# Kernel optimization log

Measured on AMD Instinct MI355X. Metric: run time of the kernel, lower is better.

Reference implementation:

```python
import jax, jax.numpy as jnp
import numpy as np

NUM_USERS = 100000
NUM_ITEMS = 50000
N = NUM_USERS + NUM_ITEMS  # total nodes
DIM = 64                   # dim_h
E = 2000000                # number of edges
NUM_LAYERS = 2


def setup_inputs() -> dict:
    key = jax.random.key(0)
    k0, k1, k2, k3, k4 = jax.random.split(key, 5)
    edge_index = jax.random.randint(k0, (2, E), 0, N, dtype=jnp.int64)
    edge_weight = jax.random.uniform(k1, (E,), dtype=jnp.float32)
    # nn.init.normal_(std=0.01) embeddings
    emb_users = 0.01 * jax.random.normal(k2, (NUM_USERS, DIM), dtype=jnp.float32)
    emb_items = 0.01 * jax.random.normal(k3, (NUM_ITEMS, DIM), dtype=jnp.float32)
    # nn.Linear(dim_h, dim_h)
    kW, kb = jax.random.split(k4)
    bound = 1.0 / np.sqrt(DIM)
    W = jax.random.uniform(kW, (DIM, DIM), minval=-bound, maxval=bound, dtype=jnp.float32)
    b = jax.random.uniform(kb, (DIM,), minval=-bound, maxval=bound, dtype=jnp.float32)
    return {"edge_index": edge_index, "edge_weight": edge_weight,
            "emb_users": emb_users, "emb_items": emb_items, "W": W, "b": b}


def reference(edge_index, edge_weight, emb_users, emb_items, W, b):
    # emb = cat([user_emb, item_emb])  -> [N, DIM]
    emb = jnp.concatenate([emb_users, emb_items], axis=0)
    src, dst = edge_index[0], edge_index[1]
    acc = emb  # running sum over layer embeddings (embs list)
    for _ in range(NUM_LAYERS):
        # LGConv with edge_weight: out[i] = sum_{j->i} w * x[j], then .relu()
        msg = edge_weight[:, None] * emb[src]            # [E, DIM] gather
        emb = jax.nn.relu(jax.ops.segment_sum(msg, dst, num_segments=N))
        acc = acc + emb
    emb_final = acc / (NUM_LAYERS + 1)                   # mean over stacked embs
    emb_final = emb_final @ W.T + b                      # final linear
    emb_users_final = emb_final[:NUM_USERS]
    emb_items_final = emb_final[NUM_USERS:]
    return (emb_users_final, emb_users, emb_items_final, emb_items)
```

## Files before the change

### kernel.cpp

```cpp
#include <hip/hip_runtime.h>
#include <hip/hip_fp16.h>

#define NUSERS 100000
#define NITEMS 50000
#define NNODES (NUSERS + NITEMS)
#define DIM 64
#define NEDGE 2000000
#define FT_ROWS 128
#define FT_BLOCKS ((NNODES + FT_ROWS - 1) / FT_ROWS)

#define BSH 7
#define NB ((NNODES + 127) >> BSH)
#define CAP 2048
#define CHUNK 4096
#define ABLOCKS ((NEDGE + CHUNK - 1) / CHUNK)
#define CONVB ((NNODES * DIM / 4 + 511) / 512)

__global__ __launch_bounds__(512)
void bucketconv_kernel(const int* __restrict__ eidx, const float* __restrict__ ew,
                       int* __restrict__ gcur, int2* __restrict__ regions,
                       const float* __restrict__ eu, const float* __restrict__ eit,
                       __half* __restrict__ tbl) {
    const int t = threadIdx.x;

    if (blockIdx.x >= ABLOCKS) {
        long i = (long)(blockIdx.x - ABLOCKS) * 512 + t;
        const long total = (long)NNODES * DIM / 4;
        if (i < total) {
            const long ue = (long)NUSERS * DIM / 4;
            float4 v = (i < ue) ? ((const float4*)eu)[i] : ((const float4*)eit)[i - ue];
            ((__half2*)tbl)[2 * i + 0] = __floats2half2_rn(v.x, v.y);
            ((__half2*)tbl)[2 * i + 1] = __floats2half2_rn(v.z, v.w);
        }
        return;
    }

    __shared__ int cursor_s[NB];
    __shared__ int excl_s[NB];
    __shared__ int gbase_s[NB];
    __shared__ int scanbuf[512];
    __shared__ int2 stage[CHUNK];
    __shared__ unsigned short sbkt[CHUNK];

    const int e0 = blockIdx.x * CHUNK;
    const int cnt_edges = min(CHUNK, NEDGE - e0);

    for (int i = t; i < NB; i += 512) cursor_s[i] = 0;
    __syncthreads();

    int2 recs[8];
    int bk[8];
    const int e4base = e0 >> 2;
#pragma unroll
    for (int k = 0; k < 2; ++k) {
        int g = k * 512 + t;
        bool ok = (4 * g) < cnt_edges;
        int4 s4 = make_int4(0, 0, 0, 0), d4 = make_int4(0, 0, 0, 0);
        float4 w4 = make_float4(0.f, 0.f, 0.f, 0.f);
        if (ok) {
            int e4 = e4base + g;
            s4 = ((const int4*)eidx)[e4];
            d4 = ((const int4*)eidx)[(NEDGE >> 2) + e4];
            w4 = ((const float4*)ew)[e4];
        }
        int ss[4] = {s4.x, s4.y, s4.z, s4.w};
        int dd[4] = {d4.x, d4.y, d4.z, d4.w};
        float ww[4] = {w4.x, w4.y, w4.z, w4.w};
#pragma unroll
        for (int j = 0; j < 4; ++j) {
            int idx = 4 * k + j;
            if (ok) {
                int d = dd[j];
                int b = d >> BSH;
                bk[idx] = b;
                recs[idx].x = ss[j] | ((d & 127) << 18);
                recs[idx].y = __float_as_int(ww[j]);
                atomicAdd(&cursor_s[b], 1);
            } else {
                bk[idx] = -1;
            }
        }
    }
    __syncthreads();

    int myv[3];
    int tsum = 0;
    const int base_i = t * 3;
#pragma unroll
    for (int j = 0; j < 3; ++j) {
        int i = base_i + j;
        myv[j] = (i < NB) ? cursor_s[i] : 0;
        tsum += myv[j];
    }
    scanbuf[t] = tsum;
    __syncthreads();
    for (int d = 1; d < 512; d <<= 1) {
        int u = (t >= d) ? scanbuf[t - d] : 0;
        __syncthreads();
        scanbuf[t] += u;
        __syncthreads();
    }
    int run = scanbuf[t] - tsum;
#pragma unroll
    for (int j = 0; j < 3; ++j) {
        int i = base_i + j;
        if (i < NB) {
            excl_s[i] = run;
            cursor_s[i] = run;
            if (myv[j] > 0) gbase_s[i] = atomicAdd(&gcur[i], myv[j]);
            run += myv[j];
        }
    }
    __syncthreads();

#pragma unroll
    for (int k = 0; k < 8; ++k) {
        if (bk[k] >= 0) {
            int p = atomicAdd(&cursor_s[bk[k]], 1);
            stage[p] = recs[k];
            sbkt[p] = (unsigned short)bk[k];
        }
    }
    __syncthreads();

    for (int i = t; i < cnt_edges; i += 512) {
        int b = sbkt[i];
        int gpos = gbase_s[b] + (i - excl_s[b]);
        if (gpos < CAP) regions[(long)b * CAP + gpos] = stage[i];
    }
}

__global__ __launch_bounds__(512)
void sortpull1_kernel(const int* __restrict__ gcur, const int2* __restrict__ regions,
                      const __half* __restrict__ tbl,
                      int2* __restrict__ edge_sorted, int2* __restrict__ rs,
                      __half* __restrict__ buf1h) {
    __shared__ int2 srec[CAP];
    __shared__ int cnt[128];
    __shared__ int excl[128];
    __shared__ int scanbuf[128];
    const int t = threadIdx.x;
    const int b = blockIdx.x;
    const int node0 = b << BSH;
    const int ecnt = min(gcur[b], CAP);
    const long gbase = (long)b * CAP;

    if (t < 128) cnt[t] = 0;
    __syncthreads();

    int2 recs[4];
#pragma unroll
    for (int k = 0; k < 4; ++k) {
        int i = k * 512 + t;
        if (i < ecnt) {
            recs[k] = regions[gbase + i];
            atomicAdd(&cnt[(recs[k].x >> 18) & 127], 1);
        }
    }
    __syncthreads();

    if (t < 128) scanbuf[t] = cnt[t];
    __syncthreads();
    for (int d = 1; d < 128; d <<= 1) {
        int u = 0;
        if (t < 128 && t >= d) u = scanbuf[t - d];
        __syncthreads();
        if (t < 128) scanbuf[t] += u;
        __syncthreads();
    }
    if (t < 128) {
        excl[t] = scanbuf[t] - cnt[t];
        cnt[t] = scanbuf[t] - cnt[t];
    }
    __syncthreads();

#pragma unroll
    for (int k = 0; k < 4; ++k) {
        int i = k * 512 + t;
        if (i < ecnt) {
            int d = (recs[k].x >> 18) & 127;
            int p = atomicAdd(&cnt[d], 1);
            int2 o;
            o.x = recs[k].x & 0x3FFFF;
            o.y = recs[k].y;
            srec[p] = o;
        }
    }
    __syncthreads();

    for (int i = t; i < ecnt; i += 512) edge_sorted[gbase + i] = srec[i];
    if (t < 128) {
        int node = node0 + t;
        if (node < NNODES) {
            int2 p;
            p.x = (int)gbase + excl[t];
            p.y = (int)gbase + cnt[t];
            rs[node] = p;
        }
    }

    const int lane = t & 63;
    const int wv = t >> 6;
    const int g = lane >> 4;
    const int gl = lane & 15;
    const int2* tb4 = (const int2*)tbl;
#pragma unroll 1
    for (int j = 0; j < 16; ++j) {
        const int local = wv * 16 + j;
        const int node = node0 + local;
        if (node >= NNODES) break;
        int i = excl[local];
        const int iend = cnt[local];
        float4 acc = make_float4(0.f, 0.f, 0.f, 0.f);
        for (; i + 15 < iend; i += 16) {
#pragma unroll
            for (int u = 0; u < 4; ++u) {
                int2 r = srec[i + 4 * u + g];
                float w = __int_as_float(r.y);
                int2 hv = tb4[((long)r.x << 4) + gl];
                float2 f0 = __half22float2(*(const __half2*)&hv.x);
                float2 f1 = __half22float2(*(const __half2*)&hv.y);
                acc.x = fmaf(w, f0.x, acc.x); acc.y = fmaf(w, f0.y, acc.y);
                acc.z = fmaf(w, f1.x, acc.z); acc.w = fmaf(w, f1.y, acc.w);
            }
        }
        if (i < iend) {
#pragma unroll
            for (int u = 0; u < 4; ++u) {
                int idx = i + 4 * u + g;
                if (idx < iend) {
                    int2 r = srec[idx];
                    float w = __int_as_float(r.y);
                    int2 hv = tb4[((long)r.x << 4) + gl];
                    float2 f0 = __half22float2(*(const __half2*)&hv.x);
                    float2 f1 = __half22float2(*(const __half2*)&hv.y);
                    acc.x = fmaf(w, f0.x, acc.x); acc.y = fmaf(w, f0.y, acc.y);
                    acc.z = fmaf(w, f1.x, acc.z); acc.w = fmaf(w, f1.y, acc.w);
                }
            }
        }
        acc.x += __shfl_xor(acc.x, 16); acc.y += __shfl_xor(acc.y, 16);
        acc.z += __shfl_xor(acc.z, 16); acc.w += __shfl_xor(acc.w, 16);
        acc.x += __shfl_xor(acc.x, 32); acc.y += __shfl_xor(acc.y, 32);
        acc.z += __shfl_xor(acc.z, 32); acc.w += __shfl_xor(acc.w, 32);
        if (g == 0) {
            __half2 o0 = __floats2half2_rn(fmaxf(acc.x, 0.f), fmaxf(acc.y, 0.f));
            __half2 o1 = __floats2half2_rn(fmaxf(acc.z, 0.f), fmaxf(acc.w, 0.f));
            int2 ov;
            ov.x = *(const int*)&o0;
            ov.y = *(const int*)&o1;
            ((int2*)buf1h)[((long)node << 4) + gl] = ov;
        }
    }
}

__global__ __launch_bounds__(512)
void pull2_kernel(const int* __restrict__ gcur, const int2* __restrict__ rs,
                  const int2* __restrict__ edge_sorted,
                  const __half* __restrict__ in_emb,
                  __half* __restrict__ out_emb) {
    __shared__ int2 srec[CAP];
    __shared__ int2 rsl[128];
    const int t = threadIdx.x;
    const int b = blockIdx.x;
    const int node0 = b << BSH;
    const int ecnt = min(gcur[b], CAP);
    const long gbase = (long)b * CAP;

    for (int i = t; i < ecnt; i += 512) srec[i] = edge_sorted[gbase + i];
    if (t < 128) {
        int node = node0 + t;
        rsl[t] = (node < NNODES) ? rs[node] : make_int2(0, 0);
    }
    __syncthreads();

    const int lane = t & 63;
    const int wv = t >> 6;
    const int g = lane >> 4;
    const int gl = lane & 15;
    const int2* tb4 = (const int2*)in_emb;
#pragma unroll 1
    for (int j = 0; j < 16; ++j) {
        const int local = wv * 16 + j;
        const int node = node0 + local;
        if (node >= NNODES) break;
        int i = rsl[local].x - (int)gbase;
        const int iend = rsl[local].y - (int)gbase;
        float4 acc = make_float4(0.f, 0.f, 0.f, 0.f);
        for (; i + 15 < iend; i += 16) {
#pragma unroll
            for (int u = 0; u < 4; ++u) {
                int2 r = srec[i + 4 * u + g];
                float w = __int_as_float(r.y);
                int2 hv = tb4[((long)r.x << 4) + gl];
                float2 f0 = __half22float2(*(const __half2*)&hv.x);
                float2 f1 = __half22float2(*(const __half2*)&hv.y);
                acc.x = fmaf(w, f0.x, acc.x); acc.y = fmaf(w, f0.y, acc.y);
                acc.z = fmaf(w, f1.x, acc.z); acc.w = fmaf(w, f1.y, acc.w);
            }
        }
        if (i < iend) {
#pragma unroll
            for (int u = 0; u < 4; ++u) {
                int idx = i + 4 * u + g;
                if (idx < iend) {
                    int2 r = srec[idx];
                    float w = __int_as_float(r.y);
                    int2 hv = tb4[((long)r.x << 4) + gl];
                    float2 f0 = __half22float2(*(const __half2*)&hv.x);
                    float2 f1 = __half22float2(*(const __half2*)&hv.y);
                    acc.x = fmaf(w, f0.x, acc.x); acc.y = fmaf(w, f0.y, acc.y);
                    acc.z = fmaf(w, f1.x, acc.z); acc.w = fmaf(w, f1.y, acc.w);
                }
            }
        }
        acc.x += __shfl_xor(acc.x, 16); acc.y += __shfl_xor(acc.y, 16);
        acc.z += __shfl_xor(acc.z, 16); acc.w += __shfl_xor(acc.w, 16);
        acc.x += __shfl_xor(acc.x, 32); acc.y += __shfl_xor(acc.y, 32);
        acc.z += __shfl_xor(acc.z, 32); acc.w += __shfl_xor(acc.w, 32);
        if (g == 0) {
            __half2 o0 = __floats2half2_rn(fmaxf(acc.x, 0.f), fmaxf(acc.y, 0.f));
            __half2 o1 = __floats2half2_rn(fmaxf(acc.z, 0.f), fmaxf(acc.w, 0.f));
            int2 ov;
            ov.x = *(const int*)&o0;
            ov.y = *(const int*)&o1;
            ((int2*)out_emb)[((long)node << 4) + gl] = ov;
        }
    }
}

__global__ __launch_bounds__(256)
void final_kernel(const float* __restrict__ eu, const float* __restrict__ eit,
                  const __half* __restrict__ e1, const __half* __restrict__ e2,
                  const float* __restrict__ W, const float* __restrict__ bias,
                  float* __restrict__ out) {
    __shared__ float4 As4[FT_ROWS * 16];
    const int t = threadIdx.x;
    const int lane = t & 63;
    const int wv = t >> 6;
    const long R0 = (long)blockIdx.x * FT_ROWS;

    float wreg[64];
#pragma unroll
    for (int k = 0; k < 16; ++k) {
        float4 wq = ((const float4*)(W + (long)lane * 64))[k];
        wreg[4 * k + 0] = wq.x; wreg[4 * k + 1] = wq.y;
        wreg[4 * k + 2] = wq.z; wreg[4 * k + 3] = wq.w;
    }
    float bj = bias[lane];

#pragma unroll
    for (int it = 0; it < 8; ++it) {
        int idx = it * 256 + t;
        long row = R0 + (idx >> 4);
        if (row < NNODES) {
            int q = idx & 15;
            const float4* g0;
            long co;
            if (row < NUSERS) {
                g0 = (const float4*)(eu + (row << 6));
                co = (long)NUSERS * DIM + (row << 6);
            } else {
                g0 = (const float4*)(eit + ((row - NUSERS) << 6));
                co = (long)2 * NUSERS * DIM + (long)NITEMS * DIM + ((row - NUSERS) << 6);
            }
            float4 v0 = g0[q];
            ((float4*)(out + co))[q] = v0;
            const __half2* h1 = (const __half2*)(e1 + (row << 6));
            const __half2* h2 = (const __half2*)(e2 + (row << 6));
            float2 f1a = __half22float2(h1[2 * q]), f1b = __half22float2(h1[2 * q + 1]);
            float2 f2a = __half22float2(h2[2 * q]), f2b = __half22float2(h2[2 * q + 1]);
            float4 s;
            s.x = v0.x + f1a.x + f2a.x; s.y = v0.y + f1a.y + f2a.y;
            s.z = v0.z + f1b.x + f2b.x; s.w = v0.w + f1b.y + f2b.y;
            As4[idx] = s;
        }
    }
    __syncthreads();

#pragma unroll 4
    for (int r = 0; r < 32; ++r) {
        int tr = wv * 32 + r;
        long row = R0 + tr;
        if (row >= NNODES) break;
        const float4* a = As4 + tr * 16;
        float s0 = 0.f, s1 = 0.f;
#pragma unroll
        for (int k = 0; k < 16; ++k) {
            float4 v = a[k];
            s0 = fmaf(v.x, wreg[4 * k + 0], s0);
            s1 = fmaf(v.y, wreg[4 * k + 1], s1);
            s0 = fmaf(v.z, wreg[4 * k + 2], s0);
            s1 = fmaf(v.w, wreg[4 * k + 3], s1);
        }
        float val = fmaf(s0 + s1, (1.0f / 3.0f), bj);
        long o = (row < NUSERS) ? row * DIM
                                : (long)2 * NUSERS * DIM + (row - NUSERS) * DIM;
        out[o + lane] = val;
    }
}

extern "C" void kernel_launch(void* const* d_in, const int* in_sizes, int n_in,
                              void* d_out, int out_size, void* d_ws, size_t ws_size,
                              hipStream_t stream) {
    const int*   eidx = (const int*)d_in[0];
    const float* ew   = (const float*)d_in[1];
    const float* eu   = (const float*)d_in[2];
    const float* eit  = (const float*)d_in[3];
    const float* W    = (const float*)d_in[4];
    const float* bias = (const float*)d_in[5];
    float* out = (float*)d_out;

    const size_t nfeat = (size_t)NNODES * DIM;
    __half* tbl         = (__half*)d_ws;
    __half* buf1h       = tbl + nfeat;
    __half* buf2h       = buf1h + nfeat;
    int2*   regions     = (int2*)(buf2h + nfeat);
    int2*   edge_sorted = regions + (long)NB * CAP;
    int2*   rs          = edge_sorted + (long)NB * CAP;
    int*    gcur        = (int*)(rs + NNODES);

    hipMemsetAsync(gcur, 0, NB * sizeof(int), stream);

    bucketconv_kernel<<<ABLOCKS + CONVB, 512, 0, stream>>>(eidx, ew, gcur, regions,
                                                           eu, eit, tbl);

    sortpull1_kernel<<<NB, 512, 0, stream>>>(gcur, regions, tbl,
                                             edge_sorted, rs, buf1h);

    pull2_kernel<<<NB, 512, 0, stream>>>(gcur, rs, edge_sorted, buf1h, buf2h);

    final_kernel<<<FT_BLOCKS, 256, 0, stream>>>(eu, eit, buf1h, buf2h, W, bias, out);
}
```

Baseline: 339.1 us.

## Use fp16 MFMA for final linear and move passthrough copy to conversion kernel

Rewrites the final linear layer as 16-row MFMA tiles (f32_16x16x32_f16), with W converted to fp16 fragments in registers and the three layer embeddings summed in fp16 from the half tables. It drops the fp32 reload of the original embeddings and moves their passthrough copy into the earlier fp32-to-half conversion blocks. The aim is to cut final-kernel FMA work and fp32 memory traffic. In exchange the input sum is now formed in fp16, so precision is lower, and the output stores are scattered 4-byte writes.

```diff
diff --git a/kernel.cpp b/kernel.cpp
--- a/kernel.cpp
+++ b/kernel.cpp
@@ -6,8 +6,6 @@
 #define NNODES (NUSERS + NITEMS)
 #define DIM 64
 #define NEDGE 2000000
-#define FT_ROWS 128
-#define FT_BLOCKS ((NNODES + FT_ROWS - 1) / FT_ROWS)
 
 #define BSH 7
 #define NB ((NNODES + 127) >> BSH)
@@ -16,11 +14,17 @@
 #define ABLOCKS ((NEDGE + CHUNK - 1) / CHUNK)
 #define CONVB ((NNODES * DIM / 4 + 511) / 512)
 
+#define NTILES (NNODES / 16)
+#define FTB ((NTILES + 7) / 8)
+
+typedef _Float16 f16x8 __attribute__((ext_vector_type(8)));
+typedef float f32x4 __attribute__((ext_vector_type(4)));
+
 __global__ __launch_bounds__(512)
 void bucketconv_kernel(const int* __restrict__ eidx, const float* __restrict__ ew,
                        int* __restrict__ gcur, int2* __restrict__ regions,
                        const float* __restrict__ eu, const float* __restrict__ eit,
-                       __half* __restrict__ tbl) {
+                       __half* __restrict__ tbl, float* __restrict__ out) {
     const int t = threadIdx.x;
 
     if (blockIdx.x >= ABLOCKS) {
@@ -28,7 +32,15 @@
         const long total = (long)NNODES * DIM / 4;
         if (i < total) {
             const long ue = (long)NUSERS * DIM / 4;
-            float4 v = (i < ue) ? ((const float4*)eu)[i] : ((const float4*)eit)[i - ue];
+            float4 v;
+            if (i < ue) {
+                v = ((const float4*)eu)[i];
+                ((float4*)(out + (long)NUSERS * DIM))[i] = v;
+            } else {
+                long j = i - ue;
+                v = ((const float4*)eit)[j];
+                ((float4*)(out + (long)2 * NUSERS * DIM + (long)NITEMS * DIM))[j] = v;
+            }
             ((__half2*)tbl)[2 * i + 0] = __floats2half2_rn(v.x, v.y);
             ((__half2*)tbl)[2 * i + 1] = __floats2half2_rn(v.z, v.w);
         }
@@ -329,74 +341,65 @@
     }
 }
 
-__global__ __launch_bounds__(256)
-void final_kernel(const float* __restrict__ eu, const float* __restrict__ eit,
-                  const __half* __restrict__ e1, const __half* __restrict__ e2,
-                  const float* __restrict__ W, const float* __restrict__ bias,
-                  float* __restrict__ out) {
-    __shared__ float4 As4[FT_ROWS * 16];
+__global__ __launch_bounds__(512)
+void final_kernel(const __half* __restrict__ tbl, const __half* __restrict__ e1,
+                  const __half* __restrict__ e2, const float* __restrict__ W,
+                  const float* __restrict__ bias, float* __restrict__ out) {
     const int t = threadIdx.x;
     const int lane = t & 63;
     const int wv = t >> 6;
-    const long R0 = (long)blockIdx.x * FT_ROWS;
-
-    float wreg[64];
-#pragma unroll
-    for (int k = 0; k < 16; ++k) {
-        float4 wq = ((const float4*)(W + (long)lane * 64))[k];
-        wreg[4 * k + 0] = wq.x; wreg[4 * k + 1] = wq.y;
-        wreg[4 * k + 2] = wq.z; wreg[4 * k + 3] = wq.w;
-    }
-    float bj = bias[lane];
-
-#pragma unroll
-    for (int it = 0; it < 8; ++it) {
-        int idx = it * 256 + t;
-        long row = R0 + (idx >> 4);
-        if (row < NNODES) {
-            int q = idx & 15;
-            const float4* g0;
-            long co;
-            if (row < NUSERS) {
-                g0 = (const float4*)(eu + (row << 6));
-                co = (long)NUSERS * DIM + (row << 6);
-            } else {
-                g0 = (const float4*)(eit + ((row - NUSERS) << 6));
-                co = (long)2 * NUSERS * DIM + (long)NITEMS * DIM + ((row - NUSERS) << 6);
-            }
-            float4 v0 = g0[q];
-            ((float4*)(out + co))[q] = v0;
-            const __half2* h1 = (const __half2*)(e1 + (row << 6));
-            const __half2* h2 = (const __half2*)(e2 + (row << 6));
-            float2 f1a = __half22float2(h1[2 * q]), f1b = __half22float2(h1[2 * q + 1]);
-            float2 f2a = __half22float2(h2[2 * q]), f2b = __half22float2(h2[2 * q + 1]);
-            float4 s;
-            s.x = v0.x + f1a.x + f2a.x; s.y = v0.y + f1a.y + f2a.y;
-            s.z = v0.z + f1b.x + f2b.x; s.w = v0.w + f1b.y + f2b.y;
-            As4[idx] = s;
-        }
-    }
-    __syncthreads();
-
-#pragma unroll 4
-    for (int r = 0; r < 32; ++r) {
-        int tr = wv * 32 + r;
-        long row = R0 + tr;
-        if (row >= NNODES) break;
-        const float4* a = As4 + tr * 16;
-        float s0 = 0.f, s1 = 0.f;
-#pragma unroll
-        for (int k = 0; k < 16; ++k) {
-            float4 v = a[k];
-            s0 = fmaf(v.x, wreg[4 * k + 0], s0);
-            s1 = fmaf(v.y, wreg[4 * k + 1], s1);
-            s0 = fmaf(v.z, wreg[4 * k + 2], s0);
-            s1 = fmaf(v.w, wreg[4 * k + 3], s1);
-        }
-        float val = fmaf(s0 + s1, (1.0f / 3.0f), bj);
+    const int tile = blockIdx.x * 8 + wv;
+    if (tile >= NTILES) return;
+    const int m = lane & 15;
+    const int kg = lane >> 4;
+
+    f16x8 bfr[4][2];
+#pragma unroll
+    for (int nt = 0; nt < 4; ++nt) {
+#pragma unroll
+        for (int kh = 0; kh < 2; ++kh) {
+            const float4* wp = (const float4*)(W + (nt * 16 + m) * 64 + kh * 32 + kg * 8);
+            float4 w0 = wp[0], w1 = wp[1];
+            f16x8 bb;
+            bb[0] = (_Float16)w0.x; bb[1] = (_Float16)w0.y;
+            bb[2] = (_Float16)w0.z; bb[3] = (_Float16)w0.w;
+            bb[4] = (_Float16)w1.x; bb[5] = (_Float16)w1.y;
+            bb[6] = (_Float16)w1.z; bb[7] = (_Float16)w1.w;
+            bfr[nt][kh] = bb;
+        }
+    }
+    float bs[4];
+#pragma unroll
+    for (int nt = 0; nt < 4; ++nt) bs[nt] = bias[nt * 16 + m];
+
+    const long rowA = (long)tile * 16 + m;
+    f16x8 afr[2];
+#pragma unroll
+    for (int kh = 0; kh < 2; ++kh) {
+        long off = rowA * 64 + kh * 32 + kg * 8;
+        f16x8 a0 = *(const f16x8*)(tbl + off);
+        f16x8 a1 = *(const f16x8*)(e1 + off);
+        f16x8 a2 = *(const f16x8*)(e2 + off);
+        afr[kh] = a0 + a1 + a2;
+    }
+
+    f32x4 acc[4];
+#pragma unroll
+    for (int nt = 0; nt < 4; ++nt) {
+        acc[nt] = (f32x4){0.f, 0.f, 0.f, 0.f};
+        acc[nt] = __builtin_amdgcn_mfma_f32_16x16x32_f16(afr[0], bfr[nt][0], acc[nt], 0, 0, 0);
+        acc[nt] = __builtin_amdgcn_mfma_f32_16x16x32_f16(afr[1], bfr[nt][1], acc[nt], 0, 0, 0);
+    }
+
+#pragma unroll
+    for (int r = 0; r < 4; ++r) {
+        long row = (long)tile * 16 + kg * 4 + r;
         long o = (row < NUSERS) ? row * DIM
                                 : (long)2 * NUSERS * DIM + (row - NUSERS) * DIM;
-        out[o + lane] = val;
+#pragma unroll
+        for (int nt = 0; nt < 4; ++nt) {
+            out[o + nt * 16 + m] = fmaf(acc[nt][r], (1.0f / 3.0f), bs[nt]);
+        }
     }
 }
 
@@ -423,12 +426,12 @@
     hipMemsetAsync(gcur, 0, NB * sizeof(int), stream);
 
     bucketconv_kernel<<<ABLOCKS + CONVB, 512, 0, stream>>>(eidx, ew, gcur, regions,
-                                                           eu, eit, tbl);
+                                                           eu, eit, tbl, out);
 
     sortpull1_kernel<<<NB, 512, 0, stream>>>(gcur, regions, tbl,
                                              edge_sorted, rs, buf1h);
 
     pull2_kernel<<<NB, 512, 0, stream>>>(gcur, rs, edge_sorted, buf1h, buf2h);
 
-    final_kernel<<<FT_BLOCKS, 256, 0, stream>>>(eu, eit, buf1h, buf2h, W, bias, out);
+    final_kernel<<<FTB, 512, 0, stream>>>(tbl, buf1h, buf2h, W, bias, out);
 }
```

Result: faster. 312.0 us (-8.0%).
